# Optimization experiments

Measured on AMD Instinct MI355X. Metric: run time of the kernel, lower is better.

## Reference

```python
import jax, jax.numpy as jnp
import numpy as np

N = 50000      # nodes
E = 800000     # edges (before self loops)
DIN = 128      # input_dim
H = 128        # hidden_dim
DOUT = 64      # output_dim
G = 64         # graphs in batch
EATTR = 16     # edge_attr dim (unused by math, kept for signature fidelity)


def _conv_params(key, din, h, scale=0.05):
    ks = jax.random.split(key, 6)
    return dict(
        lin_w=jax.random.normal(ks[0], (din, h), dtype=jnp.float32) * scale,
        lin_b=jnp.zeros((h,), jnp.float32),
        w1=jax.random.normal(ks[1], (2 * h, h), dtype=jnp.float32) * scale,
        b1=jnp.zeros((h,), jnp.float32),
        w2=jax.random.normal(ks[2], (h, h), dtype=jnp.float32) * scale,
        b2=jnp.zeros((h,), jnp.float32),
    )


def setup_inputs() -> dict:
    key = jax.random.key(0)
    ks = jax.random.split(key, 10)
    inp = {
        'x': jax.random.normal(ks[0], (N, DIN), dtype=jnp.float32),
        'edge_index': jax.random.randint(ks[1], (2, E), 0, N),
        'edge_attr': jax.random.normal(ks[2], (E, EATTR), dtype=jnp.float32),
        'batch': jnp.sort(jax.random.randint(ks[3], (N,), 0, G)),
    }
    p1 = _conv_params(ks[4], DIN, H)
    p2 = _conv_params(ks[5], H, H)
    p3 = _conv_params(ks[6], H, H)
    for i, p in enumerate((p1, p2, p3), start=1):
        for k, v in p.items():
            inp[f'c{i}_{k}'] = v
    inp['out_w'] = jax.random.normal(ks[7], (H, DOUT), dtype=jnp.float32) * 0.05
    inp['out_b'] = jnp.zeros((DOUT,), jnp.float32)
    return inp


def mpnn_conv(x, src, dst, lin_w, lin_b, w1, b1, w2, b2):
    # x: [N, din] -> h: [N, H]
    n = x.shape[0]
    h = x @ lin_w + lin_b
    loop = jnp.arange(n)
    s = jnp.concatenate([src, loop])   # x_j (source) indices, self loops appended
    d = jnp.concatenate([dst, loop])   # x_i (target) indices
    z = jnp.concatenate([h[d], h[s]], axis=-1)          # [E+N, 2H]  (cat[x_i, x_j])
    m = jax.nn.relu(z @ w1 + b1) @ w2 + b2              # [E+N, H]
    return jax.ops.segment_sum(m, d, num_segments=n)    # aggr='add' at targets


def reference(x, edge_index, edge_attr, batch,
              c1_lin_w, c1_lin_b, c1_w1, c1_b1, c1_w2, c1_b2,
              c2_lin_w, c2_lin_b, c2_w1, c2_b1, c2_w2, c2_b2,
              c3_lin_w, c3_lin_b, c3_w1, c3_b1, c3_w2, c3_b2,
              out_w, out_b):
    src, dst = edge_index[0], edge_index[1]
    h = jax.nn.relu(mpnn_conv(x, src, dst, c1_lin_w, c1_lin_b, c1_w1, c1_b1, c1_w2, c1_b2))
    h = jax.nn.relu(mpnn_conv(h, src, dst, c2_lin_w, c2_lin_b, c2_w1, c2_b1, c2_w2, c2_b2))
    h = jax.nn.relu(mpnn_conv(h, src, dst, c3_lin_w, c3_lin_b, c3_w1, c3_b1, c3_w2, c3_b2))
    # global_mean_pool over graphs
    sums = jax.ops.segment_sum(h, batch, num_segments=G)                       # [G, H]
    cnts = jax.ops.segment_sum(jnp.ones((h.shape[0],), h.dtype), batch, num_segments=G)
    pooled = sums / jnp.maximum(cnts, 1.0)[:, None]
    return pooled @ out_w + out_b
```

## Files before the change

kernel.cpp:

```cpp
#include <hip/hip_runtime.h>
#include <hip/hip_bf16.h>


typedef _Float16 f16_t;
typedef f16_t f16x2 __attribute__((ext_vector_type(2)));
typedef f16_t f16x8 __attribute__((ext_vector_type(8)));
typedef float f32x4 __attribute__((ext_vector_type(4)));
typedef float f32x2v __attribute__((ext_vector_type(2)));
typedef unsigned int u32;
typedef unsigned short u16;
typedef unsigned char u8;

__device__ __forceinline__ float f16lo(u32 v) {
    return (float)__builtin_bit_cast(f16_t, (u16)(v & 0xffff));
}
__device__ __forceinline__ float f16hi(u32 v) {
    return (float)__builtin_bit_cast(f16_t, (u16)(v >> 16));
}
__device__ __forceinline__ u16 f16b(float x) { return __builtin_bit_cast(u16, (f16_t)x); }
__device__ __forceinline__ u32 f16pack(float x, float y) {
    return (u32)f16b(x) | ((u32)f16b(y) << 16);
}

typedef __attribute__((address_space(1))) void gvoid_t;
typedef __attribute__((address_space(3))) void lvoid_t;
__device__ __forceinline__ void glds16(const void* g, void* l) {
    __builtin_amdgcn_global_load_lds((gvoid_t*)g, (lvoid_t*)l, 16, 0, 0);
}

struct PrepArgs {
    const float* x; f16_t* xb; int totalx;
    const int* ei; int E;
    int* hist; int nbk; int NB;
    const float* lin_w[3]; const float* lin_b[3];
    const float* w1[3]; const float* b1[3]; const float* w2[3];
    f16_t* linw16;
    f16_t* w1T;
    f16_t* W2t;
    float* bias256c;
};

__global__ __launch_bounds__(256) void prep_kernel(PrepArgs A, int nConvB) {
    __shared__ union { int hist[512]; u16 T16[128 * 130]; } shm;
    const int b = blockIdx.x, tid = threadIdx.x;
    const int nTr = 9, nLw = 48, nBias = 3;
    if (b < nTr) {
        int layer = b / 3, which = b % 3;
        const float* src; f16_t* dst;
        if (which == 0)      { src = A.w1[layer];          dst = A.w1T + layer * 32768; }
        else if (which == 1) { src = A.w1[layer] + 16384;  dst = A.w1T + layer * 32768 + 16384; }
        else                 { src = A.w2[layer];          dst = A.W2t + layer * 16384; }
#pragma unroll
        for (int it = 0; it < 16; ++it) {
            int idx = it * 1024 + tid * 4;
            int r = idx >> 7, c = idx & 127;
            float4 v = *(const float4*)(src + idx);
            *(u32*)&shm.T16[r * 130 + c] = f16pack(v.x, v.y);
            *(u32*)&shm.T16[r * 130 + c + 2] = f16pack(v.z, v.w);
        }
        __syncthreads();
#pragma unroll
        for (int it = 0; it < 32; ++it) {
            int o = it * 256 + tid;
            int j = o >> 6, c = (o & 63) * 2;
            u32 w = (u32)shm.T16[c * 130 + j] | ((u32)shm.T16[(c + 1) * 130 + j] << 16);
            ((u32*)dst)[o] = w;
        }
        return;
    }
    if (b < nTr + nLw) {
        int i = (b - nTr) * 1024 + tid * 4;
        int layer = i >> 14, off = i & 16383;
        float4 v = *(const float4*)(A.lin_w[layer] + off);
        *(uint2*)(A.linw16 + i) = make_uint2(f16pack(v.x, v.y), f16pack(v.z, v.w));
        return;
    }
    if (b < nTr + nLw + nBias) {
        int layer = b - nTr - nLw;
        int j = tid;
        const float* w1p = A.w1[layer];
        const float* wcol = (j < 128) ? (w1p + j) : (w1p + 16384 + (j - 128));
        const float* lbp = A.lin_b[layer];
        float s = (j < 128) ? A.b1[layer][j] : 0.f;
        for (int c = 0; c < 128; ++c) s += lbp[c] * wcol[c * 128];
        A.bias256c[layer * 256 + j] = s;
        return;
    }
    if (b < nTr + nLw + nBias + A.NB) {
        const int bb = b - nTr - nLw - nBias;
        const int nbk = A.nbk, E = A.E;
        for (int i = tid; i < nbk; i += 256) shm.hist[i] = 0;
        __syncthreads();
        const int chunk = (E + A.NB - 1) / A.NB;
        const int e0 = bb * chunk, e1 = min(E, e0 + chunk);
        for (int e = e0 + tid; e < e1; e += 256) atomicAdd(&shm.hist[A.ei[E + e] >> 7], 1);
        __syncthreads();
        for (int i = tid; i < nbk; i += 256) A.hist[(size_t)bb * nbk + i] = shm.hist[i];
        return;
    }
    int i = ((b - nTr - nLw - nBias - A.NB) * 256 + tid) * 4;
    if (i >= A.totalx) return;
    float4 v = *(const float4*)(A.x + i);
    *(uint2*)(A.xb + i) = make_uint2(f16pack(v.x, v.y), f16pack(v.z, v.w));
}

__global__ __launch_bounds__(256) void hscan_kernel(int* __restrict__ hist,
                                                    int* __restrict__ bcnt, int nbk, int NB) {
    __shared__ int sh[256];
    const int b = blockIdx.x, t = threadIdx.x;
    int run = 0;
    for (int c0 = 0; c0 < NB; c0 += 256) {
        int idx = c0 + t;
        int v = (idx < NB) ? hist[(size_t)idx * nbk + b] : 0;
        sh[t] = v;
        __syncthreads();
#pragma unroll
        for (int o = 1; o < 256; o <<= 1) {
            int u = (t >= o) ? sh[t - o] : 0;
            __syncthreads();
            sh[t] += u;
            __syncthreads();
        }
        if (idx < NB) hist[(size_t)idx * nbk + b] = run + sh[t] - v;
        int tot = sh[255];
        __syncthreads();
        run += tot;
    }
    if (t == 0) bcnt[b] = run;
}

__global__ __launch_bounds__(256) void scat_kernel(const int* __restrict__ ei,
                                                   const int* __restrict__ hist,
                                                   u32* __restrict__ bbuf, int E, int NB,
                                                   int nbk, int cap) {
    __shared__ int basep[512];
    __shared__ int cnt2[512];
    const int bb = blockIdx.x, t = threadIdx.x;
    for (int i = t; i < nbk; i += 256) {
        basep[i] = hist[(size_t)bb * nbk + i];
        cnt2[i] = 0;
    }
    __syncthreads();
    const int chunk = (E + NB - 1) / NB;
    const int e0 = bb * chunk, e1 = min(E, e0 + chunk);
    for (int e = e0 + t; e < e1; e += 256) {
        int dst = ei[E + e], src = ei[e];
        int bkt = dst >> 7;
        int r = atomicAdd(&cnt2[bkt], 1);
        int pp = basep[bkt] + r;
        if (pp < cap) bbuf[(size_t)bkt * cap + pp] = ((u32)(dst & 127) << 16) | (u32)src;
    }
}

__global__ __launch_bounds__(128) void part2_kernel(const u32* __restrict__ bbuf,
                                                    const int* __restrict__ bcnt,
                                                    int* __restrict__ row_ptr,
                                                    float* __restrict__ cntp1f,
                                                    int* __restrict__ bsumB, int cap, int N) {
    __shared__ int ldeg[128];
    __shared__ int sh[128];
    const int b = blockIdx.x, t = threadIdx.x;
    ldeg[t] = 0;
    __syncthreads();
    const int cnt = min(bcnt[b], cap);
    const u32* p = bbuf + (size_t)b * cap;
    for (int i = t; i < cnt; i += 128) atomicAdd(&ldeg[p[i] >> 16], 1);
    __syncthreads();
    int d = ldeg[t];
    sh[t] = d;
    __syncthreads();
#pragma unroll
    for (int o = 1; o < 128; o <<= 1) {
        int u = (t >= o) ? sh[t - o] : 0;
        __syncthreads();
        sh[t] += u;
        __syncthreads();
    }
    int node = (b << 7) + t;
    if (node < N) {
        row_ptr[node] = sh[t] - d;
        cntp1f[node] = (float)(d + 1);
    }
    if (t == 127) bsumB[b] = sh[127];
}

__global__ __launch_bounds__(512) void scanb_kernel(const int* __restrict__ bsumB,
                                                    int* __restrict__ bbase,
                                                    int* __restrict__ row_ptr, int nbk, int N) {
    __shared__ int sh[512];
    const int t = threadIdx.x;
    int v = (t < nbk) ? bsumB[t] : 0;
    sh[t] = v;
    __syncthreads();
#pragma unroll
    for (int o = 1; o < 512; o <<= 1) {
        int u = (t >= o) ? sh[t - o] : 0;
        __syncthreads();
        sh[t] += u;
        __syncthreads();
    }
    if (t < nbk) bbase[t] = sh[t] - v;
    if (t == 511) row_ptr[N] = sh[511];
}

__global__ __launch_bounds__(128) void part3_kernel(const u32* __restrict__ bbuf,
                                                    const int* __restrict__ bcnt,
                                                    const int* __restrict__ bbase,
                                                    int* __restrict__ row_ptr,
                                                    u16* __restrict__ colarr, int cap, int N) {
    __shared__ int lcur[128];
    const int b = blockIdx.x, t = threadIdx.x;
    const int node = (b << 7) + t;
    const int bb = bbase[b];
    int rp = 0;
    if (node < N) {
        rp = row_ptr[node] + bb;
        row_ptr[node] = rp;
    }
    lcur[t] = rp;
    __syncthreads();
    const int cnt = min(bcnt[b], cap);
    const u32* p = bbuf + (size_t)b * cap;
    for (int i = t; i < cnt; i += 128) {
        u32 en = p[i];
        int addr = atomicAdd(&lcur[en >> 16], 1);
        colarr[addr] = (u16)(en & 0xffffu);
    }
}

__device__ __forceinline__ void gemm_tile(const f16_t* __restrict__ X,
                                          const f16_t* __restrict__ Wt,
                                          f16_t* __restrict__ Y, int N,
                                          int ldc, int row0) {
    __shared__ f16_t sX[128 * 128];
    __shared__ f16_t sW[128 * 128];
    const int tid = threadIdx.x;
    const int wave = tid >> 6, lane = tid & 63;
#pragma unroll
    for (int it = 0; it < 8; ++it) {
        int idx = it * 256 + tid;
        int r = idx >> 4, c8 = idx & 15;
        int gr = row0 + r;
        if (gr >= N) gr = 0;
        glds16(X + (size_t)gr * 128 + ((c8 ^ (r & 7)) * 8),
               sX + (size_t)(it * 256 + (wave << 6)) * 8);
    }
#pragma unroll
    for (int it = 0; it < 8; ++it) {
        int idx = it * 256 + tid;
        int r = idx >> 4, c8 = idx & 15;
        glds16(Wt + (size_t)r * 128 + ((c8 ^ (r & 7)) * 8),
               sW + (size_t)(it * 256 + (wave << 6)) * 8);
    }
    __syncthreads();
    const int m = lane & 15, q = lane >> 4;
    const int sw = m & 7;
    f32x4 acc[2][8];
#pragma unroll
    for (int rt = 0; rt < 2; ++rt)
#pragma unroll
        for (int t = 0; t < 8; ++t) acc[rt][t] = (f32x4){0.f, 0.f, 0.f, 0.f};
#pragma unroll
    for (int kk = 0; kk < 4; ++kk) {
        const int g = (kk * 4 + q) ^ sw;
        f16x8 a0 = *(const f16x8*)(&sX[(wave * 32 + m) * 128 + g * 8]);
        f16x8 a1 = *(const f16x8*)(&sX[(wave * 32 + 16 + m) * 128 + g * 8]);
#pragma unroll
        for (int t = 0; t < 8; ++t) {
            f16x8 bfr = *(const f16x8*)(&sW[(t * 16 + m) * 128 + g * 8]);
            acc[0][t] = __builtin_amdgcn_mfma_f32_16x16x32_f16(a0, bfr, acc[0][t], 0, 0, 0);
            acc[1][t] = __builtin_amdgcn_mfma_f32_16x16x32_f16(a1, bfr, acc[1][t], 0, 0, 0);
        }
    }
#pragma unroll
    for (int t = 0; t < 8; ++t) {
        int col = t * 16 + m;
#pragma unroll
        for (int rt = 0; rt < 2; ++rt) {
#pragma unroll
            for (int j = 0; j < 4; ++j) {
                int r = row0 + wave * 32 + rt * 16 + q * 4 + j;
                if (r < N) Y[(size_t)r * ldc + col] = (f16_t)acc[rt][t][j];
            }
        }
    }
}

__global__ __launch_bounds__(256) void compose_kernel(const f16_t* __restrict__ w1T,
                                                      const f16_t* __restrict__ linw16,
                                                      f16_t* __restrict__ W12ct) {
    int layer = blockIdx.x >> 1, rb = blockIdx.x & 1;
    gemm_tile(w1T + layer * 32768, linw16 + layer * 16384, W12ct + layer * 32768, 256, 128,
              rb * 128);
}

template <int NT>
__global__ __launch_bounds__(512, 1) void gemm_persist(
    const f16_t* __restrict__ X, const f16_t* __restrict__ Wt,
    const float* __restrict__ bias, const float* __restrict__ bias2,
    const float* __restrict__ rowscale, f16_t* __restrict__ Y, u8* __restrict__ Y8,
    int N, int relu_flag, int ntiles) {
    __shared__ f16_t sW[NT * 16 * 128];
    __shared__ f16_t sX[2][128 * 128];
    const int tid = threadIdx.x;
    const int wave = tid >> 6, lane = tid & 63;
    const int m = lane & 15, q = lane >> 4, sw = m & 7;
    constexpr int NR = (NT == 16) ? 2 : 1;
    const int rb0 = (NT == 16) ? ((wave & 3) * 32) : (wave * 16);
    const int chalf = (NT == 16) ? (wave >> 2) : 0;

#pragma unroll
    for (int it = 0; it < NT / 2; ++it) {
        int idx = it * 512 + tid;
        int r = idx >> 4, c8 = idx & 15;
        glds16(Wt + (size_t)r * 128 + ((c8 ^ (r & 7)) * 8),
               sW + (size_t)(it * 512 + (wave << 6)) * 8);
    }
    float bvv[8], b2vv[8];
#pragma unroll
    for (int t2 = 0; t2 < 8; ++t2) {
        int colb = chalf * 128 + t2 * 16 + m;
        bvv[t2] = bias ? bias[colb] : 0.f;
        b2vv[t2] = bias2 ? bias2[colb] : 0.f;
    }
    int t = blockIdx.x;
    {
        int row0 = t * 128;
#pragma unroll
        for (int it = 0; it < 4; ++it) {
            int idx = it * 512 + tid;
            int r = idx >> 4, c8 = idx & 15;
            int gr = row0 + r;
            if (gr >= N) gr = 0;
            glds16(X + (size_t)gr * 128 + ((c8 ^ (r & 7)) * 8),
                   sX[0] + (size_t)(it * 512 + (wave << 6)) * 8);
        }
    }
    __syncthreads();
    int cur = 0;
    for (; t < ntiles; t += gridDim.x) {
        const int row0 = t * 128;
        const int tn = t + gridDim.x;
        f16_t* sXc = sX[cur];
        if (tn < ntiles) {
            const int r0n = tn * 128;
            f16_t* sXn = sX[cur ^ 1];
#pragma unroll
            for (int it = 0; it < 4; ++it) {
                int idx = it * 512 + tid;
                int r = idx >> 4, c8 = idx & 15;
                int gr = r0n + r;
                if (gr >= N) gr = 0;
                glds16(X + (size_t)gr * 128 + ((c8 ^ (r & 7)) * 8),
                       sXn + (size_t)(it * 512 + (wave << 6)) * 8);
            }
        }
        f32x4 acc[NR][8];
#pragma unroll
        for (int rt = 0; rt < NR; ++rt)
#pragma unroll
            for (int t2 = 0; t2 < 8; ++t2) acc[rt][t2] = (f32x4){0.f, 0.f, 0.f, 0.f};
#pragma unroll
        for (int kk = 0; kk < 4; ++kk) {
            const int g = (kk * 4 + q) ^ sw;
            f16x8 a0 = *(const f16x8*)(&sXc[(rb0 + m) * 128 + g * 8]);
            f16x8 a1{};
            if constexpr (NR == 2) a1 = *(const f16x8*)(&sXc[(rb0 + 16 + m) * 128 + g * 8]);
#pragma unroll
            for (int t2 = 0; t2 < 8; ++t2) {
                f16x8 bfr =
                    *(const f16x8*)(&sW[(size_t)(chalf * 128 + t2 * 16 + m) * 128 + g * 8]);
                acc[0][t2] = __builtin_amdgcn_mfma_f32_16x16x32_f16(a0, bfr, acc[0][t2], 0, 0, 0);
                if constexpr (NR == 2)
                    acc[1][t2] =
                        __builtin_amdgcn_mfma_f32_16x16x32_f16(a1, bfr, acc[1][t2], 0, 0, 0);
            }
        }
        if (NT == 16) __syncthreads();
        f16_t* region = sXc + wave * 16 * 128;
#pragma unroll
        for (int rt = 0; rt < NR; ++rt) {
            float rs[4];
#pragma unroll
            for (int j = 0; j < 4; ++j) {
                int gr = row0 + rb0 + rt * 16 + q * 4 + j;
                rs[j] = (bias2 && gr < N) ? rowscale[gr] : 0.f;
            }
#pragma unroll
            for (int t2 = 0; t2 < 8; ++t2) {
#pragma unroll
                for (int j = 0; j < 4; ++j) {
                    int rl2 = q * 4 + j;
                    float v = acc[rt][t2][j] + bvv[t2];
                    if (bias2) v += rs[j] * b2vv[t2];
                    if (relu_flag) v = fmaxf(v, 0.f);
                    region[rl2 * 128 + ((t2 * 16 + m) ^ ((rl2 & 4) << 3))] = (f16_t)v;
                }
            }
#pragma unroll
            for (int it2 = 0; it2 < 4; ++it2) {
                int i = it2 * 64 + lane;
                int rl = i >> 4, c8 = i & 15;
                int gr = row0 + rb0 + rt * 16 + rl;
                const f16_t* rp = &region[rl * 128 + ((c8 ^ (rl & 4)) * 8)];
                if (NT == 16 && chalf == 1) {
                    const u32* p = (const u32*)rp;
                    u32 lo = __builtin_amdgcn_cvt_pk_fp8_f32(f16lo(p[0]), f16hi(p[0]), 0u, false);
                    lo = __builtin_amdgcn_cvt_pk_fp8_f32(f16lo(p[1]), f16hi(p[1]), lo, true);
                    u32 hi = __builtin_amdgcn_cvt_pk_fp8_f32(f16lo(p[2]), f16hi(p[2]), 0u, false);
                    hi = __builtin_amdgcn_cvt_pk_fp8_f32(f16lo(p[3]), f16hi(p[3]), hi, true);
                    if (gr < N) *(uint2*)(Y8 + (size_t)gr * 128 + c8 * 8) = make_uint2(lo, hi);
                } else {
                    uint4 v4 = *(const uint4*)rp;
                    if (gr < N) *(uint4*)(Y + (size_t)gr * 128 + c8 * 8) = v4;
                }
            }
        }
        __syncthreads();
        cur ^= 1;
    }
}

__global__ __launch_bounds__(256) void gather_kernel(const f16_t* __restrict__ aArr,
                                                     const u8* __restrict__ b8,
                                                     const int* __restrict__ row_ptr,
                                                     const u16* __restrict__ colarr,
                                                     f16_t* __restrict__ q, int N) {
    int wid = (blockIdx.x * 256 + threadIdx.x) >> 6;
    int lane = threadIdx.x & 63;
    if (wid >= N) return;
    const int g = lane >> 4, l = lane & 15;
    uint4 A = ((const uint4*)aArr)[(size_t)wid * 16 + l];
    float a0 = f16lo(A.x), a1 = f16hi(A.x), a2 = f16lo(A.y), a3 = f16hi(A.y);
    float a4 = f16lo(A.z), a5 = f16hi(A.z), a6 = f16lo(A.w), a7 = f16hi(A.w);
    float c0 = 0.f, c1 = 0.f, c2 = 0.f, c3 = 0.f, c4 = 0.f, c5 = 0.f, c6 = 0.f, c7 = 0.f;
    const uint2* b8u = (const uint2*)b8;
    auto accum = [&](uint2 B) {
        f32x2v p0 = __builtin_amdgcn_cvt_pk_f32_fp8(B.x, false);
        f32x2v p1 = __builtin_amdgcn_cvt_pk_f32_fp8(B.x, true);
        f32x2v p2 = __builtin_amdgcn_cvt_pk_f32_fp8(B.y, false);
        f32x2v p3 = __builtin_amdgcn_cvt_pk_f32_fp8(B.y, true);
        c0 += fmaxf(a0 + p0.x, 0.f); c1 += fmaxf(a1 + p0.y, 0.f);
        c2 += fmaxf(a2 + p1.x, 0.f); c3 += fmaxf(a3 + p1.y, 0.f);
        c4 += fmaxf(a4 + p2.x, 0.f); c5 += fmaxf(a5 + p2.y, 0.f);
        c6 += fmaxf(a6 + p3.x, 0.f); c7 += fmaxf(a7 + p3.y, 0.f);
    };
    if (g == 0) accum(b8u[(size_t)wid * 16 + l]);
    int e0 = row_ptr[wid], e1 = row_ptr[wid + 1];
    int e = e0;
    for (; e + 16 <= e1; e += 16) {
        int s0 = colarr[e + g], s1 = colarr[e + 4 + g];
        int s2 = colarr[e + 8 + g], s3 = colarr[e + 12 + g];
        uint2 B0 = b8u[(size_t)s0 * 16 + l];
        uint2 B1 = b8u[(size_t)s1 * 16 + l];
        uint2 B2 = b8u[(size_t)s2 * 16 + l];
        uint2 B3 = b8u[(size_t)s3 * 16 + l];
        accum(B0); accum(B1); accum(B2); accum(B3);
    }
    for (; e < e1; e += 4) {
        int i0 = e + g;
        if (i0 < e1) accum(b8u[(size_t)colarr[i0] * 16 + l]);
    }
#pragma unroll
    for (int off = 16; off < 64; off <<= 1) {
        c0 += __shfl_xor(c0, off); c1 += __shfl_xor(c1, off);
        c2 += __shfl_xor(c2, off); c3 += __shfl_xor(c3, off);
        c4 += __shfl_xor(c4, off); c5 += __shfl_xor(c5, off);
        c6 += __shfl_xor(c6, off); c7 += __shfl_xor(c7, off);
    }
    if (g == 0) {
        uint4 o;
        o.x = f16pack(c0, c1); o.y = f16pack(c2, c3);
        o.z = f16pack(c4, c5); o.w = f16pack(c6, c7);
        ((uint4*)q)[(size_t)wid * 16 + l] = o;
    }
}

__global__ __launch_bounds__(256) void pool_kernel(const f16_t* __restrict__ agg,
                                                   const int* __restrict__ batch,
                                                   float* __restrict__ pooled,
                                                   int* __restrict__ cntg, int N) {
    int wid = (blockIdx.x * 256 + threadIdx.x) >> 6;
    int lane = threadIdx.x & 63;
    int n0 = wid * 32;
    if (n0 >= N) return;
    int n1 = min(n0 + 32, N);
    const u32* au = (const u32*)agg;
    int gcur = batch[n0];
    float sx = 0.f, sy = 0.f;
    int cnt = 0;
    for (int n = n0; n < n1; ++n) {
        int g = batch[n];
        if (g != gcur) {
            atomicAdd(&pooled[gcur * 128 + lane * 2], sx);
            atomicAdd(&pooled[gcur * 128 + lane * 2 + 1], sy);
            if (lane == 0) atomicAdd(&cntg[gcur], cnt);
            gcur = g; sx = 0.f; sy = 0.f; cnt = 0;
        }
        u32 v = au[(size_t)n * 64 + lane];
        sx += f16lo(v);
        sy += f16hi(v);
        ++cnt;
    }
    atomicAdd(&pooled[gcur * 128 + lane * 2], sx);
    atomicAdd(&pooled[gcur * 128 + lane * 2 + 1], sy);
    if (lane == 0) atomicAdd(&cntg[gcur], cnt);
}

__global__ __launch_bounds__(256) void final_kernel(const float* __restrict__ pooled,
                                                    const int* __restrict__ cntg,
                                                    const float* __restrict__ out_w,
                                                    const float* __restrict__ out_b,
                                                    float* __restrict__ out, int total) {
    int idx = blockIdx.x * 256 + threadIdx.x;
    if (idx >= total) return;
    int g = idx >> 6, o = idx & 63;
    float c = fmaxf((float)cntg[g], 1.0f);
    float s = 0.f;
#pragma unroll 4
    for (int k = 0; k < 128; ++k) s += pooled[g * 128 + k] * out_w[k * 64 + o];
    out[idx] = s / c + out_b[o];
}

extern "C" void kernel_launch(void* const* d_in, const int* in_sizes, int n_in, void* d_out,
                              int out_size, void* d_ws, size_t ws_size, hipStream_t stream) {
    const float* x = (const float*)d_in[0];
    const int* ei = (const int*)d_in[1];
    const int* batch = (const int*)d_in[3];
    const float* cw[3][6];
    for (int l = 0; l < 3; ++l)
        for (int j = 0; j < 6; ++j) cw[l][j] = (const float*)d_in[4 + l * 6 + j];
    const float* out_w = (const float*)d_in[22];
    const float* out_b = (const float*)d_in[23];
    float* out = (float*)d_out;

    const int N = in_sizes[0] / 128;
    const int E = in_sizes[1] / 2;
    const int G = out_size / 64;
    const int nbk = (N + 127) >> 7;
    const int NB = 416;
    const int cap = E / nbk + 512;

    char* base = (char*)d_ws;
    size_t off = 0;
    auto alloc = [&](size_t b) { size_t o = off; off += (b + 255) & ~(size_t)255; return o; };
    float* pooled = (float*)(base + alloc((size_t)G * 128 * 4));
    int* cntg = (int*)(base + alloc((size_t)G * 4));
    const size_t zero_bytes = off;
    int* hist = (int*)(base + alloc((size_t)NB * nbk * 4));
    int* bcnt = (int*)(base + alloc((size_t)nbk * 4));
    int* bsumB = (int*)(base + alloc((size_t)nbk * 4));
    int* bbase = (int*)(base + alloc((size_t)nbk * 4));
    int* row_ptr = (int*)(base + alloc((size_t)(N + 1) * 4));
    float* cntp1f = (float*)(base + alloc((size_t)N * 4));
    u16* colarr = (u16*)(base + alloc((size_t)E * 2));
    u32* bbuf = (u32*)(base + alloc((size_t)nbk * cap * 4));
    f16_t* xb = (f16_t*)(base + alloc((size_t)N * 128 * 2));
    f16_t* q = (f16_t*)(base + alloc((size_t)N * 128 * 2));
    f16_t* aArr = (f16_t*)(base + alloc((size_t)N * 128 * 2));
    u8* b8 = (u8*)(base + alloc((size_t)N * 128));
    f16_t* linw16 = (f16_t*)(base + alloc(3 * 16384 * 2));
    f16_t* w1T = (f16_t*)(base + alloc(3 * 32768 * 2));
    f16_t* W12ct = (f16_t*)(base + alloc(3 * 32768 * 2));
    f16_t* W2t = (f16_t*)(base + alloc(3 * 16384 * 2));
    float* bias256c = (float*)(base + alloc(3 * 256 * 4));
    (void)ws_size; (void)n_in;

    hipMemsetAsync(d_ws, 0, zero_bytes, stream);

    PrepArgs pa;
    pa.x = x; pa.xb = xb; pa.totalx = N * 128;
    pa.ei = ei; pa.E = E;
    pa.hist = hist; pa.nbk = nbk; pa.NB = NB;
    for (int l = 0; l < 3; ++l) {
        pa.lin_w[l] = cw[l][0]; pa.lin_b[l] = cw[l][1];
        pa.w1[l] = cw[l][2]; pa.b1[l] = cw[l][3]; pa.w2[l] = cw[l][4];
    }
    pa.linw16 = linw16; pa.w1T = w1T; pa.W2t = W2t; pa.bias256c = bias256c;
    const int nConvB = (N * 128 / 4 + 255) / 256;
    prep_kernel<<<9 + 48 + 3 + NB + nConvB, 256, 0, stream>>>(pa, nConvB);

    compose_kernel<<<6, 256, 0, stream>>>(w1T, linw16, W12ct);

    hscan_kernel<<<nbk, 256, 0, stream>>>(hist, bcnt, nbk, NB);
    scat_kernel<<<NB, 256, 0, stream>>>(ei, hist, bbuf, E, NB, nbk, cap);
    part2_kernel<<<nbk, 128, 0, stream>>>(bbuf, bcnt, row_ptr, cntp1f, bsumB, cap, N);
    scanb_kernel<<<1, 512, 0, stream>>>(bsumB, bbase, row_ptr, nbk, N);
    part3_kernel<<<nbk, 128, 0, stream>>>(bbuf, bcnt, bbase, row_ptr, colarr, cap, N);

    const int ntiles = (N + 127) >> 7;
    const int pgrid = (ntiles < 256) ? ntiles : 256;
    const f16_t* Xin = xb;
    for (int l = 0; l < 3; ++l) {
        gemm_persist<16><<<pgrid, 512, 0, stream>>>(Xin, W12ct + l * 32768,
                                                    bias256c + l * 256, nullptr, nullptr,
                                                    aArr, b8, N, 0, ntiles);
        gather_kernel<<<(N * 64 + 255) / 256, 256, 0, stream>>>(aArr, b8, row_ptr, colarr, q, N);
        gemm_persist<8><<<pgrid, 512, 0, stream>>>(q, W2t + l * 16384, nullptr, cw[l][5],
                                                   cntp1f, xb, nullptr, N, 1, ntiles);
        Xin = xb;
    }

    pool_kernel<<<((N + 31) / 32 * 64 + 255) / 256, 256, 0, stream>>>(Xin, batch, pooled, cntg, N);
    final_kernel<<<(G * 64 + 255) / 256, 256, 0, stream>>>(pooled, cntg, out_w, out_b, out,
                                                           G * 64);
}
```

Before: 387.8 us.

## Fuse edge gather-aggregate with second GEMM into one kernel per tile

Replaces the separate gather kernel and the persistent W2 GEMM with one kernel. Each 128-row block gathers and aggregates neighbour messages into a swizzled LDS tile, then runs MFMA against W2 held in LDS and writes the ReLU output directly. This removes the f16 q intermediate round trip to global memory and one launch per layer. In exchange it uses 64KB of LDS per block, which limits occupancy, and it loses the persistent GEMM's overlap of loads.

```diff
diff --git a/kernel.cpp b/kernel.cpp
--- a/kernel.cpp
+++ b/kernel.cpp
@@ -421,58 +421,117 @@
     }
 }
 
-__global__ __launch_bounds__(256) void gather_kernel(const f16_t* __restrict__ aArr,
-                                                     const u8* __restrict__ b8,
-                                                     const int* __restrict__ row_ptr,
-                                                     const u16* __restrict__ colarr,
-                                                     f16_t* __restrict__ q, int N) {
-    int wid = (blockIdx.x * 256 + threadIdx.x) >> 6;
-    int lane = threadIdx.x & 63;
-    if (wid >= N) return;
+__global__ __launch_bounds__(512, 4) void fused_gather_gemm8(
+    const f16_t* __restrict__ aArr, const u8* __restrict__ b8,
+    const int* __restrict__ row_ptr, const u16* __restrict__ colarr,
+    const float* __restrict__ b2, const float* __restrict__ cntp1f,
+    const f16_t* __restrict__ Wt, f16_t* __restrict__ Y, int N) {
+    __shared__ f16_t sQ[128 * 128];
+    __shared__ f16_t sW[128 * 128];
+    const int tid = threadIdx.x;
+    const int wave = tid >> 6, lane = tid & 63;
+    const int row0 = blockIdx.x * 128;
+
+#pragma unroll
+    for (int it = 0; it < 4; ++it) {
+        int idx = it * 512 + tid;
+        int r = idx >> 4, c8 = idx & 15;
+        glds16(Wt + (size_t)r * 128 + ((c8 ^ (r & 7)) * 8),
+               sW + (size_t)(it * 512 + (wave << 6)) * 8);
+    }
+
     const int g = lane >> 4, l = lane & 15;
-    uint4 A = ((const uint4*)aArr)[(size_t)wid * 16 + l];
-    float a0 = f16lo(A.x), a1 = f16hi(A.x), a2 = f16lo(A.y), a3 = f16hi(A.y);
-    float a4 = f16lo(A.z), a5 = f16hi(A.z), a6 = f16lo(A.w), a7 = f16hi(A.w);
-    float c0 = 0.f, c1 = 0.f, c2 = 0.f, c3 = 0.f, c4 = 0.f, c5 = 0.f, c6 = 0.f, c7 = 0.f;
     const uint2* b8u = (const uint2*)b8;
-    auto accum = [&](uint2 B) {
-        f32x2v p0 = __builtin_amdgcn_cvt_pk_f32_fp8(B.x, false);
-        f32x2v p1 = __builtin_amdgcn_cvt_pk_f32_fp8(B.x, true);
-        f32x2v p2 = __builtin_amdgcn_cvt_pk_f32_fp8(B.y, false);
-        f32x2v p3 = __builtin_amdgcn_cvt_pk_f32_fp8(B.y, true);
-        c0 += fmaxf(a0 + p0.x, 0.f); c1 += fmaxf(a1 + p0.y, 0.f);
-        c2 += fmaxf(a2 + p1.x, 0.f); c3 += fmaxf(a3 + p1.y, 0.f);
-        c4 += fmaxf(a4 + p2.x, 0.f); c5 += fmaxf(a5 + p2.y, 0.f);
-        c6 += fmaxf(a6 + p3.x, 0.f); c7 += fmaxf(a7 + p3.y, 0.f);
-    };
-    if (g == 0) accum(b8u[(size_t)wid * 16 + l]);
-    int e0 = row_ptr[wid], e1 = row_ptr[wid + 1];
-    int e = e0;
-    for (; e + 16 <= e1; e += 16) {
-        int s0 = colarr[e + g], s1 = colarr[e + 4 + g];
-        int s2 = colarr[e + 8 + g], s3 = colarr[e + 12 + g];
-        uint2 B0 = b8u[(size_t)s0 * 16 + l];
-        uint2 B1 = b8u[(size_t)s1 * 16 + l];
-        uint2 B2 = b8u[(size_t)s2 * 16 + l];
-        uint2 B3 = b8u[(size_t)s3 * 16 + l];
-        accum(B0); accum(B1); accum(B2); accum(B3);
-    }
-    for (; e < e1; e += 4) {
-        int i0 = e + g;
-        if (i0 < e1) accum(b8u[(size_t)colarr[i0] * 16 + l]);
-    }
-#pragma unroll
-    for (int off = 16; off < 64; off <<= 1) {
-        c0 += __shfl_xor(c0, off); c1 += __shfl_xor(c1, off);
-        c2 += __shfl_xor(c2, off); c3 += __shfl_xor(c3, off);
-        c4 += __shfl_xor(c4, off); c5 += __shfl_xor(c5, off);
-        c6 += __shfl_xor(c6, off); c7 += __shfl_xor(c7, off);
-    }
-    if (g == 0) {
-        uint4 o;
-        o.x = f16pack(c0, c1); o.y = f16pack(c2, c3);
-        o.z = f16pack(c4, c5); o.w = f16pack(c6, c7);
-        ((uint4*)q)[(size_t)wid * 16 + l] = o;
+    for (int k = 0; k < 16; ++k) {
+        const int rl = wave * 16 + k;
+        const int wid = row0 + rl;
+        if (wid >= N) {
+            if (g == 0) *(uint4*)(&sQ[rl * 128 + ((l ^ (rl & 7)) * 8)]) = make_uint4(0, 0, 0, 0);
+            continue;
+        }
+        uint4 A = ((const uint4*)aArr)[(size_t)wid * 16 + l];
+        float a0 = f16lo(A.x), a1 = f16hi(A.x), a2 = f16lo(A.y), a3 = f16hi(A.y);
+        float a4 = f16lo(A.z), a5 = f16hi(A.z), a6 = f16lo(A.w), a7 = f16hi(A.w);
+        float c0 = 0.f, c1 = 0.f, c2 = 0.f, c3 = 0.f;
+        float c4 = 0.f, c5 = 0.f, c6 = 0.f, c7 = 0.f;
+        auto accum = [&](uint2 B) {
+            f32x2v p0 = __builtin_amdgcn_cvt_pk_f32_fp8(B.x, false);
+            f32x2v p1 = __builtin_amdgcn_cvt_pk_f32_fp8(B.x, true);
+            f32x2v p2 = __builtin_amdgcn_cvt_pk_f32_fp8(B.y, false);
+            f32x2v p3 = __builtin_amdgcn_cvt_pk_f32_fp8(B.y, true);
+            c0 += fmaxf(a0 + p0.x, 0.f); c1 += fmaxf(a1 + p0.y, 0.f);
+            c2 += fmaxf(a2 + p1.x, 0.f); c3 += fmaxf(a3 + p1.y, 0.f);
+            c4 += fmaxf(a4 + p2.x, 0.f); c5 += fmaxf(a5 + p2.y, 0.f);
+            c6 += fmaxf(a6 + p3.x, 0.f); c7 += fmaxf(a7 + p3.y, 0.f);
+        };
+        if (g == 0) accum(b8u[(size_t)wid * 16 + l]);
+        const int e0 = row_ptr[wid], e1 = row_ptr[wid + 1];
+        for (int e = e0; e < e1; e += 16) {
+#pragma unroll
+            for (int s = 0; s < 4; ++s) {
+                int idx = e + s * 4 + g;
+                int src = colarr[min(idx, e1 - 1)];
+                uint2 B = b8u[(size_t)src * 16 + l];
+                if (idx < e1) accum(B);
+            }
+        }
+#pragma unroll
+        for (int off = 16; off < 64; off <<= 1) {
+            c0 += __shfl_xor(c0, off); c1 += __shfl_xor(c1, off);
+            c2 += __shfl_xor(c2, off); c3 += __shfl_xor(c3, off);
+            c4 += __shfl_xor(c4, off); c5 += __shfl_xor(c5, off);
+            c6 += __shfl_xor(c6, off); c7 += __shfl_xor(c7, off);
+        }
+        if (g == 0) {
+            uint4 o;
+            o.x = f16pack(c0, c1); o.y = f16pack(c2, c3);
+            o.z = f16pack(c4, c5); o.w = f16pack(c6, c7);
+            *(uint4*)(&sQ[rl * 128 + ((l ^ (rl & 7)) * 8)]) = o;
+        }
+    }
+    __syncthreads();
+
+    const int m = lane & 15, q = lane >> 4, sw = m & 7;
+    const int rb0 = wave * 16;
+    float b2vv[8];
+#pragma unroll
+    for (int t2 = 0; t2 < 8; ++t2) b2vv[t2] = b2[t2 * 16 + m];
+    f32x4 acc[8];
+#pragma unroll
+    for (int t2 = 0; t2 < 8; ++t2) acc[t2] = (f32x4){0.f, 0.f, 0.f, 0.f};
+#pragma unroll
+    for (int kk = 0; kk < 4; ++kk) {
+        const int gidx = (kk * 4 + q) ^ sw;
+        f16x8 a0 = *(const f16x8*)(&sQ[(rb0 + m) * 128 + gidx * 8]);
+#pragma unroll
+        for (int t2 = 0; t2 < 8; ++t2) {
+            f16x8 bfr = *(const f16x8*)(&sW[(t2 * 16 + m) * 128 + gidx * 8]);
+            acc[t2] = __builtin_amdgcn_mfma_f32_16x16x32_f16(a0, bfr, acc[t2], 0, 0, 0);
+        }
+    }
+    f16_t* region = sQ + wave * 16 * 128;
+    float rs[4];
+#pragma unroll
+    for (int j = 0; j < 4; ++j) {
+        int gr = row0 + rb0 + q * 4 + j;
+        rs[j] = (gr < N) ? cntp1f[gr] : 0.f;
+    }
+#pragma unroll
+    for (int t2 = 0; t2 < 8; ++t2) {
+#pragma unroll
+        for (int j = 0; j < 4; ++j) {
+            int rl2 = q * 4 + j;
+            float v = fmaxf(acc[t2][j] + rs[j] * b2vv[t2], 0.f);
+            region[rl2 * 128 + ((t2 * 16 + m) ^ ((rl2 & 4) << 3))] = (f16_t)v;
+        }
+    }
+#pragma unroll
+    for (int it2 = 0; it2 < 4; ++it2) {
+        int i = it2 * 64 + lane;
+        int rl = i >> 4, c8 = i & 15;
+        int gr = row0 + rb0 + rl;
+        uint4 v4 = *(const uint4*)(&region[rl * 128 + ((c8 ^ (rl & 4)) * 8)]);
+        if (gr < N) *(uint4*)(Y + (size_t)gr * 128 + c8 * 8) = v4;
     }
 }
 
@@ -564,7 +623,7 @@
     f16_t* W12ct = (f16_t*)(base + alloc(3 * 32768 * 2));
     f16_t* W2t = (f16_t*)(base + alloc(3 * 16384 * 2));
     float* bias256c = (float*)(base + alloc(3 * 256 * 4));
-    (void)ws_size; (void)n_in;
+    (void)ws_size; (void)n_in; (void)q;
 
     hipMemsetAsync(d_ws, 0, zero_bytes, stream);
 
@@ -595,9 +654,8 @@
         gemm_persist<16><<<pgrid, 512, 0, stream>>>(Xin, W12ct + l * 32768,
                                                     bias256c + l * 256, nullptr, nullptr,
                                                     aArr, b8, N, 0, ntiles);
-        gather_kernel<<<(N * 64 + 255) / 256, 256, 0, stream>>>(aArr, b8, row_ptr, colarr, q, N);
-        gemm_persist<8><<<pgrid, 512, 0, stream>>>(q, W2t + l * 16384, nullptr, cw[l][5],
-                                                   cntp1f, xb, nullptr, N, 1, ntiles);
+        fused_gather_gemm8<<<ntiles, 512, 0, stream>>>(aArr, b8, row_ptr, colarr, cw[l][5],
+                                                       cntp1f, W2t + l * 16384, xb, N);
         Xin = xb;
     }
 
```

New measurement: 507.1 us. 30.7% more time.

## Replace bucketed CSR build with global-atomic degree count and direct scatter

Applied to the files above, without the earlier changes.

The five-kernel bucketed histogram, scan and two-pass CSR construction is replaced by a global atomic degree count in the prep kernel, a per-block scan that takes its base from an atomic on a global total, and one scatter kernel that uses per-node atomic cursors. Row ranges in the gather are now taken from the row pointer plus degree, because row_ptr[N] is no longer written and rows are no longer stored in node order. The pool kernel gives each wave 8 nodes instead of 32, and the final GEMV splits the K dimension across four wave groups with a shared-memory reduction. Trade-offs: more global atomic contention on destination degrees and cursors, and a nondeterministic ordering of CSR rows and neighbour lists.

```diff
diff --git a/kernel.cpp b/kernel.cpp
--- a/kernel.cpp
+++ b/kernel.cpp
@@ -31,7 +31,7 @@
 struct PrepArgs {
     const float* x; f16_t* xb; int totalx;
     const int* ei; int E;
-    int* hist; int nbk; int NB;
+    int* deg; int NB;
     const float* lin_w[3]; const float* lin_b[3];
     const float* w1[3]; const float* b1[3]; const float* w2[3];
     f16_t* linw16;
@@ -41,7 +41,7 @@
 };
 
 __global__ __launch_bounds__(256) void prep_kernel(PrepArgs A, int nConvB) {
-    __shared__ union { int hist[512]; u16 T16[128 * 130]; } shm;
+    __shared__ u16 T16[128 * 130];
     const int b = blockIdx.x, tid = threadIdx.x;
     const int nTr = 9, nLw = 48, nBias = 3;
     if (b < nTr) {
@@ -55,15 +55,15 @@
             int idx = it * 1024 + tid * 4;
             int r = idx >> 7, c = idx & 127;
             float4 v = *(const float4*)(src + idx);
-            *(u32*)&shm.T16[r * 130 + c] = f16pack(v.x, v.y);
-            *(u32*)&shm.T16[r * 130 + c + 2] = f16pack(v.z, v.w);
+            *(u32*)&T16[r * 130 + c] = f16pack(v.x, v.y);
+            *(u32*)&T16[r * 130 + c + 2] = f16pack(v.z, v.w);
         }
         __syncthreads();
 #pragma unroll
         for (int it = 0; it < 32; ++it) {
             int o = it * 256 + tid;
             int j = o >> 6, c = (o & 63) * 2;
-            u32 w = (u32)shm.T16[c * 130 + j] | ((u32)shm.T16[(c + 1) * 130 + j] << 16);
+            u32 w = (u32)T16[c * 130 + j] | ((u32)T16[(c + 1) * 130 + j] << 16);
             ((u32*)dst)[o] = w;
         }
         return;
@@ -88,14 +88,10 @@
     }
     if (b < nTr + nLw + nBias + A.NB) {
         const int bb = b - nTr - nLw - nBias;
-        const int nbk = A.nbk, E = A.E;
-        for (int i = tid; i < nbk; i += 256) shm.hist[i] = 0;
-        __syncthreads();
+        const int E = A.E;
         const int chunk = (E + A.NB - 1) / A.NB;
         const int e0 = bb * chunk, e1 = min(E, e0 + chunk);
-        for (int e = e0 + tid; e < e1; e += 256) atomicAdd(&shm.hist[A.ei[E + e] >> 7], 1);
-        __syncthreads();
-        for (int i = tid; i < nbk; i += 256) A.hist[(size_t)bb * nbk + i] = shm.hist[i];
+        for (int e = e0 + tid; e < e1; e += 256) atomicAdd(&A.deg[A.ei[E + e]], 1);
         return;
     }
     int i = ((b - nTr - nLw - nBias - A.NB) * 256 + tid) * 4;
@@ -104,69 +100,15 @@
     *(uint2*)(A.xb + i) = make_uint2(f16pack(v.x, v.y), f16pack(v.z, v.w));
 }
 
-__global__ __launch_bounds__(256) void hscan_kernel(int* __restrict__ hist,
-                                                    int* __restrict__ bcnt, int nbk, int NB) {
-    __shared__ int sh[256];
+__global__ __launch_bounds__(128) void rowbase_kernel(const int* __restrict__ deg,
+                                                      int* __restrict__ row_ptr,
+                                                      float* __restrict__ cntp1f,
+                                                      int* __restrict__ gtot, int N) {
+    __shared__ int sh[128];
+    __shared__ int sbase;
     const int b = blockIdx.x, t = threadIdx.x;
-    int run = 0;
-    for (int c0 = 0; c0 < NB; c0 += 256) {
-        int idx = c0 + t;
-        int v = (idx < NB) ? hist[(size_t)idx * nbk + b] : 0;
-        sh[t] = v;
-        __syncthreads();
-#pragma unroll
-        for (int o = 1; o < 256; o <<= 1) {
-            int u = (t >= o) ? sh[t - o] : 0;
-            __syncthreads();
-            sh[t] += u;
-            __syncthreads();
-        }
-        if (idx < NB) hist[(size_t)idx * nbk + b] = run + sh[t] - v;
-        int tot = sh[255];
-        __syncthreads();
-        run += tot;
-    }
-    if (t == 0) bcnt[b] = run;
-}
-
-__global__ __launch_bounds__(256) void scat_kernel(const int* __restrict__ ei,
-                                                   const int* __restrict__ hist,
-                                                   u32* __restrict__ bbuf, int E, int NB,
-                                                   int nbk, int cap) {
-    __shared__ int basep[512];
-    __shared__ int cnt2[512];
-    const int bb = blockIdx.x, t = threadIdx.x;
-    for (int i = t; i < nbk; i += 256) {
-        basep[i] = hist[(size_t)bb * nbk + i];
-        cnt2[i] = 0;
-    }
-    __syncthreads();
-    const int chunk = (E + NB - 1) / NB;
-    const int e0 = bb * chunk, e1 = min(E, e0 + chunk);
-    for (int e = e0 + t; e < e1; e += 256) {
-        int dst = ei[E + e], src = ei[e];
-        int bkt = dst >> 7;
-        int r = atomicAdd(&cnt2[bkt], 1);
-        int pp = basep[bkt] + r;
-        if (pp < cap) bbuf[(size_t)bkt * cap + pp] = ((u32)(dst & 127) << 16) | (u32)src;
-    }
-}
-
-__global__ __launch_bounds__(128) void part2_kernel(const u32* __restrict__ bbuf,
-                                                    const int* __restrict__ bcnt,
-                                                    int* __restrict__ row_ptr,
-                                                    float* __restrict__ cntp1f,
-                                                    int* __restrict__ bsumB, int cap, int N) {
-    __shared__ int ldeg[128];
-    __shared__ int sh[128];
-    const int b = blockIdx.x, t = threadIdx.x;
-    ldeg[t] = 0;
-    __syncthreads();
-    const int cnt = min(bcnt[b], cap);
-    const u32* p = bbuf + (size_t)b * cap;
-    for (int i = t; i < cnt; i += 128) atomicAdd(&ldeg[p[i] >> 16], 1);
-    __syncthreads();
-    int d = ldeg[t];
+    const int node = (b << 7) + t;
+    int d = (node < N) ? deg[node] : 0;
     sh[t] = d;
     __syncthreads();
 #pragma unroll
@@ -176,55 +118,25 @@
         sh[t] += u;
         __syncthreads();
     }
-    int node = (b << 7) + t;
+    if (t == 127) sbase = atomicAdd(gtot, sh[127]);
+    __syncthreads();
     if (node < N) {
-        row_ptr[node] = sh[t] - d;
+        row_ptr[node] = sbase + sh[t] - d;
         cntp1f[node] = (float)(d + 1);
     }
-    if (t == 127) bsumB[b] = sh[127];
-}
-
-__global__ __launch_bounds__(512) void scanb_kernel(const int* __restrict__ bsumB,
-                                                    int* __restrict__ bbase,
-                                                    int* __restrict__ row_ptr, int nbk, int N) {
-    __shared__ int sh[512];
-    const int t = threadIdx.x;
-    int v = (t < nbk) ? bsumB[t] : 0;
-    sh[t] = v;
-    __syncthreads();
-#pragma unroll
-    for (int o = 1; o < 512; o <<= 1) {
-        int u = (t >= o) ? sh[t - o] : 0;
-        __syncthreads();
-        sh[t] += u;
-        __syncthreads();
-    }
-    if (t < nbk) bbase[t] = sh[t] - v;
-    if (t == 511) row_ptr[N] = sh[511];
-}
-
-__global__ __launch_bounds__(128) void part3_kernel(const u32* __restrict__ bbuf,
-                                                    const int* __restrict__ bcnt,
-                                                    const int* __restrict__ bbase,
-                                                    int* __restrict__ row_ptr,
-                                                    u16* __restrict__ colarr, int cap, int N) {
-    __shared__ int lcur[128];
-    const int b = blockIdx.x, t = threadIdx.x;
-    const int node = (b << 7) + t;
-    const int bb = bbase[b];
-    int rp = 0;
-    if (node < N) {
-        rp = row_ptr[node] + bb;
-        row_ptr[node] = rp;
-    }
-    lcur[t] = rp;
-    __syncthreads();
-    const int cnt = min(bcnt[b], cap);
-    const u32* p = bbuf + (size_t)b * cap;
-    for (int i = t; i < cnt; i += 128) {
-        u32 en = p[i];
-        int addr = atomicAdd(&lcur[en >> 16], 1);
-        colarr[addr] = (u16)(en & 0xffffu);
+}
+
+__global__ __launch_bounds__(256) void scatter_kernel(const int* __restrict__ ei,
+                                                      const int* __restrict__ row_ptr,
+                                                      int* __restrict__ cur,
+                                                      u16* __restrict__ colarr, int E, int NB) {
+    const int bb = blockIdx.x, t = threadIdx.x;
+    const int chunk = (E + NB - 1) / NB;
+    const int e0 = bb * chunk, e1 = min(E, e0 + chunk);
+    for (int e = e0 + t; e < e1; e += 256) {
+        int dst = ei[E + e], src = ei[e];
+        int pos = row_ptr[dst] + atomicAdd(&cur[dst], 1);
+        colarr[pos] = (u16)src;
     }
 }
 
@@ -424,6 +336,7 @@
 __global__ __launch_bounds__(256) void gather_kernel(const f16_t* __restrict__ aArr,
                                                      const u8* __restrict__ b8,
                                                      const int* __restrict__ row_ptr,
+                                                     const float* __restrict__ cntp1f,
                                                      const u16* __restrict__ colarr,
                                                      f16_t* __restrict__ q, int N) {
     int wid = (blockIdx.x * 256 + threadIdx.x) >> 6;
@@ -431,6 +344,8 @@
     if (wid >= N) return;
     const int g = lane >> 4, l = lane & 15;
     uint4 A = ((const uint4*)aArr)[(size_t)wid * 16 + l];
+    int e0 = row_ptr[wid];
+    int e1 = e0 + (int)cntp1f[wid] - 1;
     float a0 = f16lo(A.x), a1 = f16hi(A.x), a2 = f16lo(A.y), a3 = f16hi(A.y);
     float a4 = f16lo(A.z), a5 = f16hi(A.z), a6 = f16lo(A.w), a7 = f16hi(A.w);
     float c0 = 0.f, c1 = 0.f, c2 = 0.f, c3 = 0.f, c4 = 0.f, c5 = 0.f, c6 = 0.f, c7 = 0.f;
@@ -446,7 +361,6 @@
         c6 += fmaxf(a6 + p3.x, 0.f); c7 += fmaxf(a7 + p3.y, 0.f);
     };
     if (g == 0) accum(b8u[(size_t)wid * 16 + l]);
-    int e0 = row_ptr[wid], e1 = row_ptr[wid + 1];
     int e = e0;
     for (; e + 16 <= e1; e += 16) {
         int s0 = colarr[e + g], s1 = colarr[e + 4 + g];
@@ -482,9 +396,9 @@
                                                    int* __restrict__ cntg, int N) {
     int wid = (blockIdx.x * 256 + threadIdx.x) >> 6;
     int lane = threadIdx.x & 63;
-    int n0 = wid * 32;
+    int n0 = wid * 8;
     if (n0 >= N) return;
-    int n1 = min(n0 + 32, N);
+    int n1 = min(n0 + 8, N);
     const u32* au = (const u32*)agg;
     int gcur = batch[n0];
     float sx = 0.f, sy = 0.f;
@@ -511,15 +425,23 @@
                                                     const int* __restrict__ cntg,
                                                     const float* __restrict__ out_w,
                                                     const float* __restrict__ out_b,
-                                                    float* __restrict__ out, int total) {
-    int idx = blockIdx.x * 256 + threadIdx.x;
-    if (idx >= total) return;
-    int g = idx >> 6, o = idx & 63;
-    float c = fmaxf((float)cntg[g], 1.0f);
+                                                    float* __restrict__ out) {
+    __shared__ float red[256];
+    const int g = blockIdx.x, tid = threadIdx.x;
+    const int o = tid & 63, part = tid >> 6;
     float s = 0.f;
-#pragma unroll 4
-    for (int k = 0; k < 128; ++k) s += pooled[g * 128 + k] * out_w[k * 64 + o];
-    out[idx] = s / c + out_b[o];
+#pragma unroll
+    for (int kk = 0; kk < 32; ++kk) {
+        int k = part * 32 + kk;
+        s += pooled[g * 128 + k] * out_w[k * 64 + o];
+    }
+    red[tid] = s;
+    __syncthreads();
+    if (part == 0) {
+        float c = fmaxf((float)cntg[g], 1.0f);
+        float tot = red[o] + red[o + 64] + red[o + 128] + red[o + 192];
+        out[g * 64 + o] = tot / c + out_b[o];
+    }
 }
 
 extern "C" void kernel_launch(void* const* d_in, const int* in_sizes, int n_in, void* d_out,
@@ -539,22 +461,19 @@
     const int G = out_size / 64;
     const int nbk = (N + 127) >> 7;
     const int NB = 416;
-    const int cap = E / nbk + 512;
 
     char* base = (char*)d_ws;
     size_t off = 0;
     auto alloc = [&](size_t b) { size_t o = off; off += (b + 255) & ~(size_t)255; return o; };
     float* pooled = (float*)(base + alloc((size_t)G * 128 * 4));
     int* cntg = (int*)(base + alloc((size_t)G * 4));
+    int* deg = (int*)(base + alloc((size_t)N * 4));
+    int* curp = (int*)(base + alloc((size_t)N * 4));
+    int* gtot = (int*)(base + alloc(256));
     const size_t zero_bytes = off;
-    int* hist = (int*)(base + alloc((size_t)NB * nbk * 4));
-    int* bcnt = (int*)(base + alloc((size_t)nbk * 4));
-    int* bsumB = (int*)(base + alloc((size_t)nbk * 4));
-    int* bbase = (int*)(base + alloc((size_t)nbk * 4));
     int* row_ptr = (int*)(base + alloc((size_t)(N + 1) * 4));
     float* cntp1f = (float*)(base + alloc((size_t)N * 4));
     u16* colarr = (u16*)(base + alloc((size_t)E * 2));
-    u32* bbuf = (u32*)(base + alloc((size_t)nbk * cap * 4));
     f16_t* xb = (f16_t*)(base + alloc((size_t)N * 128 * 2));
     f16_t* q = (f16_t*)(base + alloc((size_t)N * 128 * 2));
     f16_t* aArr = (f16_t*)(base + alloc((size_t)N * 128 * 2));
@@ -571,7 +490,7 @@
     PrepArgs pa;
     pa.x = x; pa.xb = xb; pa.totalx = N * 128;
     pa.ei = ei; pa.E = E;
-    pa.hist = hist; pa.nbk = nbk; pa.NB = NB;
+    pa.deg = deg; pa.NB = NB;
     for (int l = 0; l < 3; ++l) {
         pa.lin_w[l] = cw[l][0]; pa.lin_b[l] = cw[l][1];
         pa.w1[l] = cw[l][2]; pa.b1[l] = cw[l][3]; pa.w2[l] = cw[l][4];
@@ -582,11 +501,8 @@
 
     compose_kernel<<<6, 256, 0, stream>>>(w1T, linw16, W12ct);
 
-    hscan_kernel<<<nbk, 256, 0, stream>>>(hist, bcnt, nbk, NB);
-    scat_kernel<<<NB, 256, 0, stream>>>(ei, hist, bbuf, E, NB, nbk, cap);
-    part2_kernel<<<nbk, 128, 0, stream>>>(bbuf, bcnt, row_ptr, cntp1f, bsumB, cap, N);
-    scanb_kernel<<<1, 512, 0, stream>>>(bsumB, bbase, row_ptr, nbk, N);
-    part3_kernel<<<nbk, 128, 0, stream>>>(bbuf, bcnt, bbase, row_ptr, colarr, cap, N);
+    rowbase_kernel<<<nbk, 128, 0, stream>>>(deg, row_ptr, cntp1f, gtot, N);
+    scatter_kernel<<<NB, 256, 0, stream>>>(ei, row_ptr, curp, colarr, E, NB);
 
     const int ntiles = (N + 127) >> 7;
     const int pgrid = (ntiles < 256) ? ntiles : 256;
@@ -595,13 +511,13 @@
         gemm_persist<16><<<pgrid, 512, 0, stream>>>(Xin, W12ct + l * 32768,
                                                     bias256c + l * 256, nullptr, nullptr,
                                                     aArr, b8, N, 0, ntiles);
-        gather_kernel<<<(N * 64 + 255) / 256, 256, 0, stream>>>(aArr, b8, row_ptr, colarr, q, N);
+        gather_kernel<<<(N * 64 + 255) / 256, 256, 0, stream>>>(aArr, b8, row_ptr, cntp1f,
+                                                                colarr, q, N);
         gemm_persist<8><<<pgrid, 512, 0, stream>>>(q, W2t + l * 16384, nullptr, cw[l][5],
                                                    cntp1f, xb, nullptr, N, 1, ntiles);
         Xin = xb;
     }
 
-    pool_kernel<<<((N + 31) / 32 * 64 + 255) / 256, 256, 0, stream>>>(Xin, batch, pooled, cntg, N);
-    final_kernel<<<(G * 64 + 255) / 256, 256, 0, stream>>>(pooled, cntg, out_w, out_b, out,
-                                                           G * 64);
-}
+    pool_kernel<<<((N + 7) / 8 * 64 + 255) / 256, 256, 0, stream>>>(Xin, batch, pooled, cntg, N);
+    final_kernel<<<G, 256, 0, stream>>>(pooled, cntg, out_w, out_b, out);
+}
```

Result: slower. 434.6 us (+12.1%).
